# Kernel tuning notes

Measured on AMD Instinct MI355X. Metric: run time of the kernel, lower is better.

The kernel has to match this reference:

```python
import jax, jax.numpy as jnp
import numpy as np

N, E, D, H, C = 50000, 1600000, 256, 8, 32

def setup_inputs() -> dict:
    key = jax.random.key(0)
    ks = jax.random.split(key, 7)
    feat = jax.random.normal(ks[0], (N, D), dtype=jnp.float32)
    edge_weight = jax.random.uniform(ks[1], (E,), dtype=jnp.float32)
    W_lin = jax.random.normal(ks[2], (D, H * C), dtype=jnp.float32) * (1.0 / np.sqrt(D))
    att_l = jax.random.normal(ks[3], (1, H, C), dtype=jnp.float32) * (1.0 / np.sqrt(H))
    att_r = jax.random.normal(ks[4], (1, H, C), dtype=jnp.float32) * (1.0 / np.sqrt(H))
    W_res = jax.random.normal(ks[5], (D, H * C), dtype=jnp.float32) * (1.0 / np.sqrt(D))
    edge_index = jax.random.randint(ks[6], (2, E), 0, N, dtype=jnp.int32)
    return {"feat": feat, "edge_weight": edge_weight, "W_lin": W_lin,
            "att_l": att_l, "att_r": att_r, "W_res": W_res, "edge_index": edge_index}

def reference(feat, edge_weight, W_lin, att_l, att_r, W_res, edge_index):
    n_nodes = feat.shape[0]
    h, c = att_l.shape[1], att_l.shape[2]
    src, dst = edge_index[0], edge_index[1]
    # node projection: [N, H, C]
    x = (feat @ W_lin).reshape(n_nodes, h, c)
    alpha_l = (x * att_l).sum(-1)  # [N, H]
    alpha_r = (x * att_r).sum(-1)  # [N, H]
    # per-edge scores [E, H]
    alpha = alpha_l[src] + alpha_r[dst]
    alpha = edge_weight[:, None] * alpha
    alpha = jnp.where(alpha > 0, alpha, 0.2 * alpha)  # leaky_relu(0.2)
    # segment softmax over destination nodes
    amax = jax.lax.stop_gradient(jax.ops.segment_max(alpha, dst, num_segments=n_nodes))
    ex = jnp.exp(alpha - amax[dst])
    denom = jax.ops.segment_sum(ex, dst, num_segments=n_nodes)
    coeff = ex / (denom[dst] + 1e-16)  # [E, H]
    # weighted message aggregation
    msg = x[src] * coeff[:, :, None]  # [E, H, C]
    agg = jax.ops.segment_sum(msg, dst, num_segments=n_nodes)  # [N, H, C]
    out = jax.nn.elu(agg).reshape(n_nodes, h * c)
    out = out + feat @ W_res  # residual
    return out
```

## Files before the change

### kernel.cpp

```cpp
#include <hip/hip_runtime.h>
#include <stdint.h>

#define D_DIM 256
#define NPAD  640
#define NSH   8

typedef __bf16 bf16x8 __attribute__((ext_vector_type(8)));
typedef float  f32x4  __attribute__((ext_vector_type(4)));

__device__ __forceinline__ float bf2f(unsigned short u) {
  union { unsigned int i; float f; } cv; cv.i = ((unsigned int)u) << 16; return cv.f;
}
__device__ __forceinline__ unsigned short f2bf(float f) {
  union { float f; unsigned int i; } cv; cv.f = f;
  unsigned int i = cv.i;
  unsigned int lsb = (i >> 16) & 1u;
  i += 0x7fffu + lsb;
  return (unsigned short)(i >> 16);
}
__device__ __forceinline__ void gld16(const void* gptr, void* lptr) {
  __builtin_amdgcn_global_load_lds(
      (const __attribute__((address_space(1))) unsigned int*)gptr,
      (__attribute__((address_space(3))) unsigned int*)lptr, 16, 0, 0);
}

__global__ __launch_bounds__(256) void setup_cvt_prep(
    const float* __restrict__ feat, unsigned short* __restrict__ fb,
    const float* __restrict__ W_lin, const float* __restrict__ W_res,
    const float* __restrict__ att_l, const float* __restrict__ att_r,
    unsigned short* __restrict__ Bt, int nelem, int nb_cvt) {
  int bid = blockIdx.x, t = threadIdx.x;
  if (bid < nb_cvt) {
    int i = (bid * 256 + t) * 8;
    if (i >= nelem) return;
    float4 v0 = *(const float4*)(feat + i);
    float4 v1 = *(const float4*)(feat + i + 4);
    ushort4 a, b;
    a.x = f2bf(v0.x); a.y = f2bf(v0.y); a.z = f2bf(v0.z); a.w = f2bf(v0.w);
    b.x = f2bf(v1.x); b.y = f2bf(v1.y); b.z = f2bf(v1.z); b.w = f2bf(v1.w);
    *(ushort4*)(fb + i) = a;
    *(ushort4*)(fb + i + 4) = b;
  } else {
    int idx = (bid - nb_cvt) * 256 + t;
    int n = idx >> 8, k = idx & 255;
    float v = 0.f;
    if (n < 256) v = W_lin[k * 256 + n];
    else if (n < 512) v = W_res[k * 256 + (n - 256)];
    else if (n < 520) {
      int h = n - 512; float s = 0.f;
      #pragma unroll
      for (int c = 0; c < 32; ++c) s += W_lin[k * 256 + h * 32 + c] * att_l[h * 32 + c];
      v = s;
    } else if (n < 528) {
      int h = n - 520; float s = 0.f;
      #pragma unroll
      for (int c = 0; c < 32; ++c) s += W_lin[k * 256 + h * 32 + c] * att_r[h * 32 + c];
      v = s;
    }
    Bt[idx] = f2bf(v);
  }
}

__global__ __launch_bounds__(256) void scan_partial(const int* __restrict__ cntS,
                                                    int* __restrict__ bsum, int N, int Np) {
  __shared__ int s[256];
  int t = threadIdx.x;
  int i = blockIdx.x * 256 + t;
  int v = 0;
  if (i < N) {
    #pragma unroll
    for (int sh = 0; sh < NSH; ++sh) v += cntS[sh * Np + i];
  }
  s[t] = v;
  __syncthreads();
  for (int off = 128; off > 0; off >>= 1) {
    if (t < off) s[t] += s[t + off];
    __syncthreads();
  }
  if (t == 0) bsum[blockIdx.x] = s[0];
}

__global__ __launch_bounds__(256) void scan_apply(const int* __restrict__ cntS,
                                                  const int* __restrict__ bsum,
                                                  int* __restrict__ row_ptr,
                                                  int* __restrict__ soffA, int N, int Np) {
  __shared__ int red[256];
  __shared__ int s[256];
  int t = threadIdx.x;
  int b = blockIdx.x;
  int acc = 0;
  for (int j = t; j < b; j += 256) acc += bsum[j];
  red[t] = acc;
  __syncthreads();
  for (int off = 128; off > 0; off >>= 1) {
    if (t < off) red[t] += red[t + off];
    __syncthreads();
  }
  int base = red[0];

  int i = b * 256 + t;
  int c[NSH]; int v = 0;
  if (i < N) {
    #pragma unroll
    for (int sh = 0; sh < NSH; ++sh) { c[sh] = cntS[sh * Np + i]; v += c[sh]; }
  }
  s[t] = v;
  __syncthreads();
  for (int off = 1; off < 256; off <<= 1) {
    int u = (t >= off) ? s[t - off] : 0;
    __syncthreads();
    s[t] += u;
    __syncthreads();
  }
  int excl = base + s[t] - v;
  if (i < N) {
    row_ptr[i] = excl;
    int run = excl;
    #pragma unroll
    for (int sh = 0; sh < NSH; ++sh) { soffA[sh * Np + i] = run; run += c[sh]; }
    if (i == N - 1) row_ptr[N] = excl + v;
  }
}

__global__ __launch_bounds__(256) void gemm_hist(
    const unsigned short* __restrict__ A,
    const unsigned short* __restrict__ Bt,
    float* __restrict__ out, unsigned short* __restrict__ xbf,
    float* __restrict__ alpha_l, float* __restrict__ alpha_r, int M, int gx,
    const int* __restrict__ dst, int* __restrict__ cntS, int* __restrict__ rank,
    int E, int Np, int echunk) {
  __shared__ unsigned short As[128 * 64];
  __shared__ unsigned short Bs[128 * 64];

  int tid  = threadIdx.x;
  int bid  = (int)blockIdx.x;
  int grp  = bid / 6, pos = bid - grp * 6;

  if (pos == 5) {
    int ebase = grp * echunk;
    int elim  = ebase + echunk; if (elim > E) elim = E;
    for (int eb = ebase; eb < elim; eb += 4096) {
      #pragma unroll
      for (int u = 0; u < 16; ++u) {
        int e = eb + u * 256 + tid;
        if (e < elim) {
          int d = dst[e];
          rank[e] = atomicAdd(&cntS[(e & (NSH - 1)) * Np + d], 1);
        }
      }
    }
    return;
  }

  int w    = tid >> 6, lane = tid & 63;
  int gb   = grp * 5 + pos;

  int ng   = gx * 5;
  int q    = ng >> 3, r = ng & 7;
  int xcd  = gb & 7, j = gb >> 3;
  int wg   = (xcd < r ? xcd * (q + 1) : r * (q + 1) + (xcd - r) * q) + j;

  int nbn  = NPAD / 128;
  int bm   = (wg / nbn) * 128, bn = (wg % nbn) * 128;
  int wm   = (w & 1) * 64, wn = (w >> 1) * 64;
  int l16  = lane & 15, quad = lane >> 4;

  f32x4 acc[4][4] = {};

  int sr8     = lane >> 3;
  int koff_sw = (((lane & 7) ^ sr8) * 8);

  for (int k0 = 0; k0 < 256; k0 += 64) {
    #pragma unroll
    for (int jj = 0; jj < 4; ++jj) {
      int rbase = w * 32 + jj * 8;
      int rga = bm + rbase + sr8; if (rga > M - 1) rga = M - 1;
      gld16(A  + (size_t)rga * 256 + k0 + koff_sw, &As[rbase * 64]);
      gld16(Bt + (size_t)(bn + rbase + sr8) * 256 + k0 + koff_sw, &Bs[rbase * 64]);
    }
    __syncthreads();
    #pragma unroll
    for (int kk = 0; kk < 64; kk += 32) {
      bf16x8 a[4], b[4];
      #pragma unroll
      for (int mi = 0; mi < 4; ++mi) {
        int rr = wm + mi * 16 + l16;
        int col = (kk * 2 + quad * 16) ^ ((rr & 7) << 4);
        a[mi] = *(const bf16x8*)((const char*)&As[rr * 64] + col);
      }
      #pragma unroll
      for (int ni = 0; ni < 4; ++ni) {
        int rr = wn + ni * 16 + l16;
        int col = (kk * 2 + quad * 16) ^ ((rr & 7) << 4);
        b[ni] = *(const bf16x8*)((const char*)&Bs[rr * 64] + col);
      }
      #pragma unroll
      for (int mi = 0; mi < 4; ++mi)
        #pragma unroll
        for (int ni = 0; ni < 4; ++ni)
          acc[mi][ni] = __builtin_amdgcn_mfma_f32_16x16x32_bf16(a[mi], b[ni], acc[mi][ni], 0, 0, 0);
    }
    __syncthreads();
  }

  #pragma unroll
  for (int mi = 0; mi < 4; ++mi) {
    #pragma unroll
    for (int rr = 0; rr < 4; ++rr) {
      int row = bm + wm + mi * 16 + quad * 4 + rr;
      if (row >= M) continue;
      #pragma unroll
      for (int ni = 0; ni < 4; ++ni) {
        int n = bn + wn + ni * 16 + l16;
        float v = acc[mi][ni][rr];
        if (n < 256)      xbf[(size_t)row * 256 + n] = f2bf(v);
        else if (n < 512) out[(size_t)row * 256 + (n - 256)] = v;
        else if (n < 520) alpha_l[row * 8 + (n - 512)] = v;
        else if (n < 528) alpha_r[row * 8 + (n - 520)] = v;
      }
    }
  }
}

__global__ __launch_bounds__(256) void scatter_kernel(
    const int* __restrict__ eidx, const float* __restrict__ ew,
    const int* __restrict__ soffA, const int* __restrict__ rank,
    int2* __restrict__ pairs, int E, int Np) {
  int e = blockIdx.x * 256 + threadIdx.x;
  if (e < E) {
    int d = eidx[E + e];
    int pos = soffA[(e & (NSH - 1)) * Np + d] + rank[e];
    int2 p; p.x = eidx[e]; p.y = __float_as_int(ew[e]);
    pairs[pos] = p;
  }
}

__global__ __launch_bounds__(256) void agg_kernel(
    const int* __restrict__ row_ptr, const int2* __restrict__ pairs,
    const float* __restrict__ alpha_l, const float* __restrict__ alpha_r,
    const unsigned short* __restrict__ xbf, float* __restrict__ out, int N) {
  __shared__ float red[2][64][6];
  int nin  = threadIdx.x >> 7;
  int wv   = (threadIdx.x >> 6) & 1;
  int lane = threadIdx.x & 63;
  int node = blockIdx.x * 2 + nin;
  bool active = node < N;
  int h  = lane >> 3;
  int cb = lane << 2;

  float l = 0.f, ac0 = 0.f, ac1 = 0.f, ac2 = 0.f, ac3 = 0.f;

  if (active) {
    int beg = row_ptr[node], end = row_ptr[node + 1];
    if (beg < end) {
      float arv = alpha_r[node * 8 + h];
      int last = end - 1;
      const unsigned short* xb = xbf + cb;
      for (int jg = beg + wv * 4; jg < end; jg += 8) {
        int2 q[4];
        #pragma unroll
        for (int u = 0; u < 4; ++u) {
          int t = jg + u; t = (t < last) ? t : last;
          q[u] = pairs[t];
        }
        float al[4];
        #pragma unroll
        for (int u = 0; u < 4; ++u) al[u] = alpha_l[(size_t)q[u].x * 8 + h];
        ushort4 xv[4];
        #pragma unroll
        for (int u = 0; u < 4; ++u)
          xv[u] = *(const ushort4*)(xb + ((size_t)q[u].x << 8));
        #pragma unroll
        for (int u = 0; u < 4; ++u) {
          float a = __int_as_float(q[u].y) * (al[u] + arv);
          a = (a > 0.f) ? a : 0.2f * a;
          float p = __expf(a);
          p = (jg + u < end) ? p : 0.f;
          l += p;
          ac0 = fmaf(p, bf2f(xv[u].x), ac0);
          ac1 = fmaf(p, bf2f(xv[u].y), ac1);
          ac2 = fmaf(p, bf2f(xv[u].z), ac2);
          ac3 = fmaf(p, bf2f(xv[u].w), ac3);
        }
      }
    }
  }

  if (wv == 1) {
    red[nin][lane][0] = l;
    red[nin][lane][1] = ac0; red[nin][lane][2] = ac1;
    red[nin][lane][3] = ac2; red[nin][lane][4] = ac3;
  }
  __syncthreads();
  if (active && wv == 0) {
    l   += red[nin][lane][0];
    ac0 += red[nin][lane][1]; ac1 += red[nin][lane][2];
    ac2 += red[nin][lane][3]; ac3 += red[nin][lane][4];
    float r = 1.0f / (l + 1e-16f);
    float o0 = ac0 * r, o1 = ac1 * r, o2 = ac2 * r, o3 = ac3 * r;
    o0 = (o0 > 0.f) ? o0 : expm1f(o0);
    o1 = (o1 > 0.f) ? o1 : expm1f(o1);
    o2 = (o2 > 0.f) ? o2 : expm1f(o2);
    o3 = (o3 > 0.f) ? o3 : expm1f(o3);
    float4* op = (float4*)(out + ((size_t)node << 8) + cb);
    float4 res = *op;
    res.x += o0; res.y += o1; res.z += o2; res.w += o3;
    *op = res;
  }
}

extern "C" void kernel_launch(void* const* d_in, const int* in_sizes, int n_in,
                              void* d_out, int out_size, void* d_ws, size_t ws_size,
                              hipStream_t stream) {
  const float* feat  = (const float*)d_in[0];
  const float* ew    = (const float*)d_in[1];
  const float* W_lin = (const float*)d_in[2];
  const float* att_l = (const float*)d_in[3];
  const float* att_r = (const float*)d_in[4];
  const float* W_res = (const float*)d_in[5];
  const int*   eidx  = (const int*)d_in[6];
  float* out = (float*)d_out;

  int N = in_sizes[0] / D_DIM;
  int E = in_sizes[1];
  int Np = (N + 255) & ~255;

  char* p = (char*)d_ws;
  auto alloc = [&](size_t bytes) {
    char* r = p; p += (bytes + 255) & ~(size_t)255; return r;
  };
  unsigned short* xbf  = (unsigned short*)alloc((size_t)N * 256 * 2);
  unsigned short* fb   = (unsigned short*)alloc((size_t)N * 256 * 2);
  float* alpha_l       = (float*)alloc((size_t)N * 8 * 4);
  float* alpha_r       = (float*)alloc((size_t)N * 8 * 4);
  unsigned short* Bt   = (unsigned short*)alloc((size_t)NPAD * D_DIM * 2);
  int*   row_ptr       = (int*)alloc((size_t)(N + 1) * 4);
  int*   cntS          = (int*)alloc((size_t)NSH * Np * 4);
  int*   soffA         = (int*)alloc((size_t)NSH * Np * 4);
  int*   rank          = (int*)alloc((size_t)E * 4);
  int*   bsum          = (int*)alloc(1024);
  int2*  pairs_sep     = (int2*)alloc((size_t)E * 8);
  bool sep_ok = ((size_t)((char*)(pairs_sep + E) - (char*)d_ws) <= ws_size);
  int2* pairs = sep_ok ? pairs_sep : (int2*)fb;

  int nb      = (N + 255) / 256;
  int nb_cvt  = (N * 256 / 8 + 255) / 256;
  int nb_prep = NPAD * D_DIM / 256;
  int nb_scat = (E + 255) / 256;
  int gx = (N + 127) / 128;
  int echunk = (E + gx - 1) / gx;

  hipMemsetAsync(cntS, 0, (size_t)NSH * Np * 4, stream);

  setup_cvt_prep<<<nb_cvt + nb_prep, 256, 0, stream>>>(
      feat, fb, W_lin, W_res, att_l, att_r, Bt, N * 256, nb_cvt);

  gemm_hist<<<gx * 6, 256, 0, stream>>>(
      fb, Bt, out, xbf, alpha_l, alpha_r, N, gx,
      eidx + E, cntS, rank, E, Np, echunk);

  scan_partial<<<nb, 256, 0, stream>>>(cntS, bsum, N, Np);
  scan_apply<<<nb, 256, 0, stream>>>(cntS, bsum, row_ptr, soffA, N, Np);

  scatter_kernel<<<nb_scat, 256, 0, stream>>>(eidx, ew, soffA, rank, pairs, E, Np);

  agg_kernel<<<(N + 1) / 2, 256, 0, stream>>>(row_ptr, pairs, alpha_l, alpha_r, xbf, out, N);
}
```

Baseline: 394.6 us.

## Move histogram into setup kernel and overlap edge scatter with GEMM

The dst histogram/rank atomics move from the GEMM kernel into the setup conversion kernel as extra blocks. The GEMM kernel's sixth block per group now does the edge scatter into CSR order, which can run because the scans have already run. That removes the standalone scatter launch and hides scatter traffic behind GEMM compute. The risk is that the histogram atomics now sit on the setup kernel's critical path, and scatter blocks compete with GEMM blocks for bandwidth. When pairs would alias the fb buffer, the fused scatter is disabled and the old scatter kernel runs instead.

```diff
diff --git a/kernel.cpp b/kernel.cpp
--- a/kernel.cpp
+++ b/kernel.cpp
@@ -24,12 +24,27 @@
       (__attribute__((address_space(3))) unsigned int*)lptr, 16, 0, 0);
 }
 
-__global__ __launch_bounds__(256) void setup_cvt_prep(
+__global__ __launch_bounds__(256) void setup_fused(
     const float* __restrict__ feat, unsigned short* __restrict__ fb,
     const float* __restrict__ W_lin, const float* __restrict__ W_res,
     const float* __restrict__ att_l, const float* __restrict__ att_r,
-    unsigned short* __restrict__ Bt, int nelem, int nb_cvt) {
+    unsigned short* __restrict__ Bt, int nelem, int nb_hist, int nb_cvt,
+    const int* __restrict__ dst, int* __restrict__ cntS, int* __restrict__ rank,
+    int E, int Np) {
   int bid = blockIdx.x, t = threadIdx.x;
+  if (bid < nb_hist) {
+    int base = bid * 2048 + t;
+    #pragma unroll
+    for (int u = 0; u < 8; ++u) {
+      int e = base + u * 256;
+      if (e < E) {
+        int d = dst[e];
+        rank[e] = atomicAdd(&cntS[(e & (NSH - 1)) * Np + d], 1);
+      }
+    }
+    return;
+  }
+  bid -= nb_hist;
   if (bid < nb_cvt) {
     int i = (bid * 256 + t) * 8;
     if (i >= nelem) return;
@@ -122,13 +137,14 @@
   }
 }
 
-__global__ __launch_bounds__(256) void gemm_hist(
+__global__ __launch_bounds__(256) void gemm_scatter(
     const unsigned short* __restrict__ A,
     const unsigned short* __restrict__ Bt,
     float* __restrict__ out, unsigned short* __restrict__ xbf,
     float* __restrict__ alpha_l, float* __restrict__ alpha_r, int M, int gx,
-    const int* __restrict__ dst, int* __restrict__ cntS, int* __restrict__ rank,
-    int E, int Np, int echunk) {
+    const int* __restrict__ eidx, const float* __restrict__ ew,
+    const int* __restrict__ soffA, const int* __restrict__ rank,
+    int2* __restrict__ pairs, int E, int Np, int echunk, int fuse) {
   __shared__ unsigned short As[128 * 64];
   __shared__ unsigned short Bs[128 * 64];
 
@@ -137,15 +153,18 @@
   int grp  = bid / 6, pos = bid - grp * 6;
 
   if (pos == 5) {
+    if (!fuse) return;
     int ebase = grp * echunk;
     int elim  = ebase + echunk; if (elim > E) elim = E;
-    for (int eb = ebase; eb < elim; eb += 4096) {
-      #pragma unroll
-      for (int u = 0; u < 16; ++u) {
+    for (int eb = ebase; eb < elim; eb += 2048) {
+      #pragma unroll
+      for (int u = 0; u < 8; ++u) {
         int e = eb + u * 256 + tid;
         if (e < elim) {
-          int d = dst[e];
-          rank[e] = atomicAdd(&cntS[(e & (NSH - 1)) * Np + d], 1);
+          int s = eidx[e], d = eidx[E + e];
+          int p2 = soffA[(e & (NSH - 1)) * Np + d] + rank[e];
+          int2 pr; pr.x = s; pr.y = __float_as_int(ew[e]);
+          pairs[p2] = pr;
         }
       }
     }
@@ -342,27 +361,31 @@
   int2*  pairs_sep     = (int2*)alloc((size_t)E * 8);
   bool sep_ok = ((size_t)((char*)(pairs_sep + E) - (char*)d_ws) <= ws_size);
   int2* pairs = sep_ok ? pairs_sep : (int2*)fb;
+  int fuse = sep_ok ? 1 : 0;
 
   int nb      = (N + 255) / 256;
   int nb_cvt  = (N * 256 / 8 + 255) / 256;
   int nb_prep = NPAD * D_DIM / 256;
+  int nb_hist = (E + 2047) / 2048;
   int nb_scat = (E + 255) / 256;
   int gx = (N + 127) / 128;
   int echunk = (E + gx - 1) / gx;
 
   hipMemsetAsync(cntS, 0, (size_t)NSH * Np * 4, stream);
 
-  setup_cvt_prep<<<nb_cvt + nb_prep, 256, 0, stream>>>(
-      feat, fb, W_lin, W_res, att_l, att_r, Bt, N * 256, nb_cvt);
-
-  gemm_hist<<<gx * 6, 256, 0, stream>>>(
-      fb, Bt, out, xbf, alpha_l, alpha_r, N, gx,
-      eidx + E, cntS, rank, E, Np, echunk);
+  setup_fused<<<nb_hist + nb_cvt + nb_prep, 256, 0, stream>>>(
+      feat, fb, W_lin, W_res, att_l, att_r, Bt, N * 256, nb_hist, nb_cvt,
+      eidx + E, cntS, rank, E, Np);
 
   scan_partial<<<nb, 256, 0, stream>>>(cntS, bsum, N, Np);
   scan_apply<<<nb, 256, 0, stream>>>(cntS, bsum, row_ptr, soffA, N, Np);
 
-  scatter_kernel<<<nb_scat, 256, 0, stream>>>(eidx, ew, soffA, rank, pairs, E, Np);
+  gemm_scatter<<<gx * 6, 256, 0, stream>>>(
+      fb, Bt, out, xbf, alpha_l, alpha_r, N, gx,
+      eidx, ew, soffA, rank, pairs, E, Np, echunk, fuse);
+
+  if (!fuse)
+    scatter_kernel<<<nb_scat, 256, 0, stream>>>(eidx, ew, soffA, rank, pairs, E, Np);
 
   agg_kernel<<<(N + 1) / 2, 256, 0, stream>>>(row_ptr, pairs, alpha_l, alpha_r, xbf, out, N);
 }
```

Result: slower. 434.5 us (+10.1%).
